# Kernel tuning notes

Hardware: AMD Instinct MI355X
Metric: run time of the kernel (lower is better)

Reference implementation:

```python
import jax, jax.numpy as jnp
import numpy as np

N, D, K = 8192, 512, 15  # points, embed dim, k_neighbors
EPS_MEAN = 1e-8
EPS_NORM = 1e-8


def _knn(emb, k):
    sq_norms = jnp.sum(emb * emb, axis=1)
    sq = sq_norms[:, None] + sq_norms[None, :] - 2.0 * (emb @ emb.T)
    sq = jnp.maximum(sq, 0.0)
    # smallest k+1 distances (squared dist is monotone in dist); slot 0 is self (dist 0)
    neg_vals, idx = jax.lax.top_k(-sq, k + 1)
    knn_sq = -neg_vals[:, 1:]
    knn_idx = idx[:, 1:]
    knn_d = jnp.sqrt(jnp.maximum(knn_sq, 1e-12))
    return knn_d, knn_idx


def _curvature_signature(knn_d):
    mean_d = jnp.mean(knn_d, axis=1, keepdims=True) + EPS_MEAN
    return jnp.sort(knn_d / mean_d, axis=1)


def _angular_signature(emb, knn_idx):
    k = knn_idx.shape[1]
    nb = emb[knn_idx]                      # [N, k, D] neighbor gather
    v = nb - emb[:, None, :]               # [N, k, D]
    nrm = jnp.linalg.norm(v, axis=2, keepdims=True)
    v = v / jnp.maximum(nrm, EPS_NORM)     # F.normalize semantics
    cos = jnp.einsum('nkd,nld->nkl', v, v)  # [N, k, k] batched small GEMM
    iu, ju = np.triu_indices(k, 1)
    ang = cos[:, iu, ju]                   # [N, k(k-1)/2]
    return jnp.sort(ang, axis=1)


def setup_inputs() -> dict:
    key = jax.random.key(0)
    k1, k2 = jax.random.split(key)
    embeddings = jax.random.normal(k1, (N, D), dtype=jnp.float32)
    # reference signatures computed from a perturbed copy (realistic set_reference)
    ref_emb = embeddings + 0.1 * jax.random.normal(k2, (N, D), dtype=jnp.float32)
    ref_d, ref_idx = _knn(ref_emb, K)
    reference_curvature_sig = _curvature_signature(ref_d)
    reference_angular_sig = _angular_signature(ref_emb, ref_idx)
    return {
        'embeddings': embeddings,
        'reference_curvature_sig': reference_curvature_sig,
        'reference_angular_sig': reference_angular_sig,
    }


def reference(embeddings, reference_curvature_sig, reference_angular_sig):
    n = embeddings.shape[0]
    k = min(K, n - 1)
    knn_d, knn_idx = _knn(embeddings, k)
    curr_curv = _curvature_signature(knn_d)          # [N, k]
    curr_ang = _angular_signature(embeddings, knn_idx)  # [N, k(k-1)/2]
    ref_curv = reference_curvature_sig[:n, :k]
    ref_ang = reference_angular_sig[:n]
    curv_loss = jnp.mean((curr_curv - ref_curv) ** 2)
    m = min(curr_ang.shape[1], ref_ang.shape[1])
    ang_loss = jnp.mean((curr_ang[:, :m] - ref_ang[:, :m]) ** 2)
    return 0.3 * curv_loss + 0.7 * ang_loss
```

## Files before the change

### kernel.cpp

```cpp
#include <hip/hip_runtime.h>
#include <hip/hip_bf16.h>
#include <math.h>

#define NPTS  8192
#define DIM   512
#define KNNK  15
#define NCAND 22
#define NPAIR 105
#define CINF  3.0e38f
#define EMPTYK 0xFFFFFFFFu
#define TAU_MARGIN (3u << 16)

#define NI      128
#define NJSPLIT 16
#define NJ      (NPTS/NJSPLIT)
#define JS      128
#define NSUB    (NJ/JS)
#define BK      32
#define NCH     (DIM/BK)
#define SDW     68
#define NLIST   NJSPLIT
#define NKEYS   (NLIST * KNNK)

#define BUF0_OFF   0
#define BUF1_OFF   16384
#define SQJ_OFF    34816
#define KNN_LDS    39936

typedef __attribute__((ext_vector_type(8))) short short8;
typedef __attribute__((ext_vector_type(4))) float f32x4;
typedef unsigned int uint32;

static __device__ __forceinline__ float wave_sum_f(float v) {
#pragma unroll
  for (int m = 32; m > 0; m >>= 1) v += __shfl_xor(v, m, 64);
  return v;
}

static __device__ __forceinline__ void load_lds16(const void* g, void* l) {
  __builtin_amdgcn_global_load_lds(
      (const __attribute__((address_space(1))) void*)g,
      (__attribute__((address_space(3))) void*)l, 16, 0, 0);
}

static __device__ __forceinline__ void bf16split(float x, short& h, short& l) {
  __hip_bfloat16 hb = __float2bfloat16(x);
  const float hf = __bfloat162float(hb);
  __hip_bfloat16 lb = __float2bfloat16(x - hf);
  h = *(short*)&hb;
  l = *(short*)&lb;
}

static __device__ __forceinline__ int lanes_below(unsigned long long B) {
  int c = __builtin_amdgcn_mbcnt_lo((uint32)B, 0);
  return __builtin_amdgcn_mbcnt_hi((uint32)(B >> 32), c);
}

static __device__ __forceinline__ void chain15(uint32 (&td)[15], uint32 c) {
#pragma unroll
  for (int p = 0; p < 15; ++p) {
    const uint32 lo = min(c, td[p]);
    const uint32 hi = max(c, td[p]);
    td[p] = lo; c = hi;
  }
}

#define PUSHK(k_) { const uint32 kv_ = (k_); \
  p0=(nc==0)?kv_:p0;  p1=(nc==1)?kv_:p1;  p2=(nc==2)?kv_:p2; \
  p3=(nc==3)?kv_:p3;  p4=(nc==4)?kv_:p4;  p5=(nc==5)?kv_:p5; \
  p6=(nc==6)?kv_:p6;  p7=(nc==7)?kv_:p7;  p8=(nc==8)?kv_:p8; \
  p9=(nc==9)?kv_:p9;  p10=(nc==10)?kv_:p10; p11=(nc==11)?kv_:p11; \
  ++nc; }

#define DRAINALL { \
  if (__any(nc >  0)) { if (nc >  0) chain15(td, p0);  } \
  if (__any(nc >  1)) { if (nc >  1) chain15(td, p1);  } \
  if (__any(nc >  2)) { if (nc >  2) chain15(td, p2);  } \
  if (__any(nc >  3)) { if (nc >  3) chain15(td, p3);  } \
  if (__any(nc >  4)) { if (nc >  4) chain15(td, p4);  } \
  if (__any(nc >  5)) { if (nc >  5) chain15(td, p5);  } \
  if (__any(nc >  6)) { if (nc >  6) chain15(td, p6);  } \
  if (__any(nc >  7)) { if (nc >  7) chain15(td, p7);  } \
  if (__any(nc >  8)) { if (nc >  8) chain15(td, p8);  } \
  if (__any(nc >  9)) { if (nc >  9) chain15(td, p9);  } \
  if (__any(nc > 10)) { if (nc > 10) chain15(td, p10); } \
  if (__any(nc > 11)) { if (nc > 11) chain15(td, p11); } \
  nc = 0; guard = min(tau_cur, td[14]); }

__global__ __launch_bounds__(256) void prep_kernel(
    const float* __restrict__ E, float* __restrict__ sqn,
    ushort* __restrict__ EA, ushort* __restrict__ EB,
    uint32* __restrict__ tauk) {
  const int row  = blockIdx.x * 4 + (threadIdx.x >> 6);
  const int lane = threadIdx.x & 63;
  const float SR2 = 1.4142135623730951f;
  float s = 0.f;
#pragma unroll
  for (int c = 0; c < 8; ++c) {
    const int d0 = lane + 64 * c;
    const float x = E[(size_t)row * DIM + d0];
    s = fmaf(x, x, s);
    __hip_bfloat16 ha = __float2bfloat16(-SR2 * x);
    __hip_bfloat16 hb = __float2bfloat16( SR2 * x);
    EA[(size_t)row * DIM + d0] = *(ushort*)&ha;
    EB[(size_t)row * DIM + d0] = *(ushort*)&hb;
  }
  s = wave_sum_f(s);
  if (lane == 0) { sqn[row] = s; tauk[row] = EMPTYK; }
}

__global__ __launch_bounds__(256, 4) void knn_kernel(
    const ushort* __restrict__ EA, const ushort* __restrict__ EB,
    const float* __restrict__ sqn, uint32* __restrict__ tauk,
    uint32* __restrict__ knnk) {
  __shared__ __align__(16) char sm[KNN_LDS];
  uint32* sdp  = (uint32*)sm;
  float*  sqjs = (float*)(sm + SQJ_OFF);

  const int tid = threadIdx.x;
  const int w   = tid >> 6;
  const int L   = tid & 63;
  const int wr  = (w >> 1) & 1;
  const int wc  = w & 1;
  const int i0  = blockIdx.x * NI;
  const int jsplit = blockIdx.y;
  const int j0  = jsplit * NJ;

  if (tid < NJ / 4) ((float4*)sqjs)[tid] = ((const float4*)(sqn + j0))[tid];

  const ushort* gsrc = (w < 2) ? EA : EB;
  const int lrow  = L >> 2;
  const int swz_k = ((L & 3) ^ ((L >> 3) & 3)) * 8;
  const int lds_woff = ((w < 2) ? 0 : 8192) + (w & 1) * 4096;
  const int slot8 = (((L >> 4) ^ ((L >> 1) & 3)) * 8);

  const int myrow = tid >> 1;
  const int h     = tid & 1;
  const int gi    = i0 + myrow;

  uint32 td[15];
#pragma unroll
  for (int p = 0; p < 15; ++p) td[p] = EMPTYK;

  __syncthreads();

  for (int js = 0; js < NSUB; ++js) {
    const int jrow0 = j0 + js * JS;
    const int trowW = ((w < 2) ? i0 : jrow0) + (w & 1) * 64;
    const ushort* gbase = gsrc + (size_t)(trowW + lrow) * DIM + swz_k;

    f32x4 acc[4][4];
#pragma unroll
    for (int fj = 0; fj < 4; ++fj) {
      const f32x4 sq = *(const f32x4*)&sqjs[js * 128 + wc * 64 + fj * 16 + (L >> 4) * 4];
#pragma unroll
      for (int fi = 0; fi < 4; ++fi) acc[fj][fi] = sq;
    }

    {
      char* lp = sm + BUF0_OFF + lds_woff;
#pragma unroll
      for (int s = 0; s < 4; ++s)
        load_lds16(gbase + (size_t)(s * 16) * DIM, lp + s * 1024);
    }
    __syncthreads();

#pragma unroll 2
    for (int ch = 0; ch < NCH; ++ch) {
      const int cb  = (ch & 1) ? BUF1_OFF : BUF0_OFF;
      const int nbo = (ch & 1) ? BUF0_OFF : BUF1_OFF;
      if (ch < NCH - 1) {
        char* lp = sm + nbo + lds_woff;
        const ushort* gp = gbase + (ch + 1) * BK;
#pragma unroll
        for (int s = 0; s < 4; ++s)
          load_lds16(gp + (size_t)(s * 16) * DIM, lp + s * 1024);
      }

      const ushort* sA = (const ushort*)(sm + cb);
      const ushort* sB = (const ushort*)(sm + cb + 8192);

      short8 a[4], b[4];
#pragma unroll
      for (int f = 0; f < 4; ++f) {
        a[f] = *(const short8*)&sA[(wr * 64 + f * 16 + (L & 15)) * BK + slot8];
        b[f] = *(const short8*)&sB[(wc * 64 + f * 16 + (L & 15)) * BK + slot8];
      }
#pragma unroll
      for (int fj = 0; fj < 4; ++fj)
#pragma unroll
        for (int fi = 0; fi < 4; ++fi)
          acc[fj][fi] = __builtin_amdgcn_mfma_f32_16x16x32_bf16(b[fj], a[fi], acc[fj][fi], 0, 0, 0);
      __syncthreads();
    }

#pragma unroll
    for (int fj = 0; fj < 4; ++fj)
#pragma unroll
      for (int fi = 0; fi < 4; ++fi) {
        const int i_t = wr * 64 + fi * 16 + (L & 15);
        const int jd  = wc * 32 + fj * 8 + (L >> 4) * 2;
        uint32 dw0, dw1;
        asm("v_cvt_pk_bf16_f32 %0, %1, %2" : "=v"(dw0) : "v"(acc[fj][fi][0]), "v"(acc[fj][fi][1]));
        asm("v_cvt_pk_bf16_f32 %0, %1, %2" : "=v"(dw1) : "v"(acc[fj][fi][2]), "v"(acc[fj][fi][3]));
        uint2 d2; d2.x = dw0; d2.y = dw1;
        *(uint2*)&sdp[i_t * SDW + jd] = d2;
      }
    __syncthreads();

    const uint32 tau_cur = __hip_atomic_load(&tauk[gi], __ATOMIC_RELAXED,
                                             __HIP_MEMORY_SCOPE_AGENT);
    const int selfc = gi - jrow0;
    if (selfc >= 0 && selfc < JS && h == (selfc >> 6))
      *(ushort*)(sm + myrow * (SDW * 4) + selfc * 2) = 0x7F80;

    const uint32* rowp = sdp + myrow * SDW + 32 * h;
    const uint32 jb = (uint32)(jrow0 + 64 * h);
    uint32 guard = min(tau_cur, td[14]);
    uint32 nc = 0;
    uint32 p0=0,p1=0,p2=0,p3=0,p4=0,p5=0,p6=0,p7=0,p8=0,p9=0,p10=0,p11=0;

#pragma unroll 2
    for (int q = 0; q < 8; ++q) {
      const uint4 pv = *(const uint4*)&rowp[4 * q];
      const uint32 jq = jb + 8 * q;
      uint32 kx;
      kx = (pv.x << 16)          | (jq + 0); if (kx < guard) PUSHK(kx);
      kx = (pv.x & 0xFFFF0000u)  | (jq + 1); if (kx < guard) PUSHK(kx);
      kx = (pv.y << 16)          | (jq + 2); if (kx < guard) PUSHK(kx);
      kx = (pv.y & 0xFFFF0000u)  | (jq + 3); if (kx < guard) PUSHK(kx);
      kx = (pv.z << 16)          | (jq + 4); if (kx < guard) PUSHK(kx);
      kx = (pv.z & 0xFFFF0000u)  | (jq + 5); if (kx < guard) PUSHK(kx);
      kx = (pv.w << 16)          | (jq + 6); if (kx < guard) PUSHK(kx);
      kx = (pv.w & 0xFFFF0000u)  | (jq + 7); if (kx < guard) PUSHK(kx);
      if (__any(nc >= 4)) { DRAINALL; }
    }
    if (__any(nc > 0)) { DRAINALL; }

    if (td[14] < 0x7F000000u) atomicMin(&tauk[gi], td[14] + TAU_MARGIN);
    __syncthreads();
  }

  uint32* mdk = (uint32*)sm;
#pragma unroll
  for (int p = 0; p < 15; ++p) mdk[(myrow * 2 + h) * 15 + p] = td[p];
  __syncthreads();
  if (h == 0) {
    const uint32* la = &mdk[(myrow * 2 + 0) * 15];
    const uint32* lb = &mdk[(myrow * 2 + 1) * 15];
    int pa = 0, pb = 0;
    const size_t base = ((size_t)gi * NLIST + jsplit) * KNNK;
    for (int s = 0; s < KNNK; ++s) {
      const uint32 va = la[pa], vb = lb[pb];
      uint32 v;
      if (va <= vb) { v = va; ++pa; } else { v = vb; ++pb; }
      knnk[base + s] = v;
    }
  }
}

__global__ __launch_bounds__(256) void sig_kernel(
    const float* __restrict__ E, const uint32* __restrict__ knnk,
    const float* __restrict__ refc, const float* __restrict__ refa,
    float2* __restrict__ pacc) {
  __shared__ float gsm[4][352];

  const int tid = threadIdx.x;
  const int wid = tid >> 6;
  const int L   = tid & 63;
  const int i   = blockIdx.x * 4 + wid;

  const uint32* kl = knnk + (size_t)i * NKEYS;
  const uint32 k0 = kl[L];
  const uint32 k1 = kl[L + 64];
  const uint32 k2 = kl[L + 128];
  const uint32 k3 = (L < NKEYS - 192) ? kl[L + 192] : EMPTYK;

  uint32 T = 0;
  for (int b = 31; b >= 0; --b) {
    const uint32 Tt = T | (1u << b);
    const int cnt = __popcll(__ballot(k0 < Tt)) + __popcll(__ballot(k1 < Tt)) +
                    __popcll(__ballot(k2 < Tt)) + __popcll(__ballot(k3 < Tt));
    if (cnt <= NCAND - 1) T = Tt;
  }

  uint32* candL = (uint32*)&gsm[wid][288];
  {
    const unsigned long long B0 = __ballot(k0 <= T);
    const unsigned long long B1 = __ballot(k1 <= T);
    const unsigned long long B2 = __ballot(k2 <= T);
    const unsigned long long B3 = __ballot(k3 <= T);
    int off = 0;
    if (k0 <= T) candL[off + lanes_below(B0)] = k0;
    off += __popcll(B0);
    if (k1 <= T) candL[off + lanes_below(B1)] = k1;
    off += __popcll(B1);
    if (k2 <= T) candL[off + lanes_below(B2)] = k2;
    off += __popcll(B2);
    if (k3 <= T) candL[off + lanes_below(B3)] = k3;
  }
  asm volatile("s_waitcnt lgkmcnt(0)" ::: "memory");
  const uint32 cand_key = (L < NCAND) ? candL[L] : EMPTYK;
  int cand_nb = ((cand_key >> 16) < 0x7F80u) ? (int)(cand_key & 0x1FFFu) : i;

  const float* Ei = E + (size_t)i * DIM;
  const int u = L & 7;
  const int g = L >> 3;
  float sr[3];
#pragma unroll
  for (int r = 0; r < 3; ++r) {
    const int c = r * 8 + g;
    const int row = __shfl(cand_nb, c, 64);
    const float4* r4 = (const float4*)(E + (size_t)row * DIM);
    const float4* e4 = (const float4*)Ei;
    float a0 = 0.f, a1 = 0.f, a2 = 0.f, a3 = 0.f;
#pragma unroll
    for (int t = 0; t < 16; ++t) {
      const float4 av = r4[u + 8 * t];
      const float4 ev = e4[u + 8 * t];
      const float d0 = av.x - ev.x, d1 = av.y - ev.y;
      const float d2 = av.z - ev.z, d3 = av.w - ev.w;
      a0 = fmaf(d0, d0, a0); a1 = fmaf(d1, d1, a1);
      a2 = fmaf(d2, d2, a2); a3 = fmaf(d3, d3, a3);
    }
    float s = (a0 + a1) + (a2 + a3);
    s += __shfl_xor(s, 1, 64);
    s += __shfl_xor(s, 2, 64);
    s += __shfl_xor(s, 4, 64);
    sr[r] = s;
  }
  const int srcl = (L & 7) * 8;
  const float t0 = __shfl(sr[0], srcl, 64);
  const float t1 = __shfl(sr[1], srcl, 64);
  const float t2 = __shfl(sr[2], srcl, 64);
  float csq = (L >> 3) == 0 ? t0 : ((L >> 3) == 1 ? t1 : t2);
  if (L >= NCAND || cand_nb == i) csq = CINF;

  int rank = 0;
#pragma unroll
  for (int j = 0; j < NCAND; ++j) {
    const float vj = __shfl(csq, j, 64);
    rank += (vj < csq) || (vj == csq && j < L);
  }
  float* dselL = &gsm[wid][312];
  int*   nbrL  = (int*)&gsm[wid][328];
  if (L < NCAND && rank < KNNK) { dselL[rank] = csq; nbrL[rank] = cand_nb; }
  asm volatile("s_waitcnt lgkmcnt(0)" ::: "memory");
  const int sel = L & 15;
  const int mynb = (sel < KNNK) ? nbrL[sel] : i;
  const float myd = (L < KNNK) ? sqrtf(fmaxf(dselL[L], 1e-12f)) : 0.f;

  float curvs;
  {
    float dd = (L < KNNK) ? myd : 0.f;
    float tot = wave_sum_f(dd);
    float mean_d = tot / (float)KNNK + 1e-8f;
    float diff = (L < KNNK) ? (dd / mean_d - refc[i * KNNK + L]) : 0.f;
    curvs = wave_sum_f(diff * diff);
  }

  const float4* nb4 = (const float4*)(E + (size_t)mynb * DIM);
  const float4* ei4 = (const float4*)Ei;
  const int qo = (L >> 4) * 2;

  f32x4 gH, gX1, gX2;
#pragma unroll
  for (int r = 0; r < 4; ++r) { gH[r] = 0.f; gX1[r] = 0.f; gX2[r] = 0.f; }

#pragma unroll
  for (int c = 0; c < 16; ++c) {
    const float4 f0 = nb4[qo + c * 8];
    const float4 f1 = nb4[qo + 1 + c * 8];
    const float4 g0 = ei4[qo + c * 8];
    const float4 g1 = ei4[qo + 1 + c * 8];
    float v[8];
    v[0] = f0.x - g0.x; v[1] = f0.y - g0.y; v[2] = f0.z - g0.z; v[3] = f0.w - g0.w;
    v[4] = f1.x - g1.x; v[5] = f1.y - g1.y; v[6] = f1.z - g1.z; v[7] = f1.w - g1.w;
    short8 ah, al;
#pragma unroll
    for (int q = 0; q < 8; ++q) {
      short hh, ll;
      bf16split(v[q], hh, ll);
      ah[q] = hh; al[q] = ll;
    }
    gH  = __builtin_amdgcn_mfma_f32_16x16x32_bf16(ah, ah, gH, 0, 0, 0);
    gX1 = __builtin_amdgcn_mfma_f32_16x16x32_bf16(ah, al, gX1, 0, 0, 0);
    gX2 = __builtin_amdgcn_mfma_f32_16x16x32_bf16(al, ah, gX2, 0, 0, 0);
  }

#pragma unroll
  for (int q = 0; q < 4; ++q)
    gsm[wid][((L >> 4) * 4 + q) * 17 + (L & 15)] = gH[q] + gX1[q] + gX2[q];
  asm volatile("s_waitcnt lgkmcnt(0)" ::: "memory");

  if (L < 16) {
    const float dv = gsm[wid][L * 17 + L];
    const float nrm = sqrtf(fmaxf(dv, 0.f));
    gsm[wid][272 + L] = 1.0f / fmaxf(nrm, 1e-8f);
  }
  asm volatile("s_waitcnt lgkmcnt(0)" ::: "memory");

  float c0 = CINF, c1 = CINF;
#pragma unroll
  for (int s = 0; s < 2; ++s) {
    const int p = L + 64 * s;
    if (p < NPAIR) {
      int a = 0, rem = p, cnt = 14;
      while (rem >= cnt) { rem -= cnt; --cnt; ++a; }
      const int b = a + 1 + rem;
      const float cv = gsm[wid][a * 17 + b] * gsm[wid][272 + a] * gsm[wid][272 + b];
      if (s == 0) c0 = cv; else c1 = cv;
    }
  }

#pragma unroll
  for (int k = 2; k <= 128; k <<= 1) {
#pragma unroll
    for (int j = k >> 1; j >= 1; j >>= 1) {
      const bool dir = ((L & (k >> 1)) == 0);
      if (j == 1) {
        const float lo = fminf(c0, c1), hi = fmaxf(c0, c1);
        c0 = dir ? lo : hi;
        c1 = dir ? hi : lo;
      } else {
        const int m = j >> 1;
        const float o0 = __shfl_xor(c0, m, 64);
        const float o1 = __shfl_xor(c1, m, 64);
        const bool lower = ((L & m) == 0);
        c0 = (lower == dir) ? fminf(c0, o0) : fmaxf(c0, o0);
        c1 = (lower == dir) ? fminf(c1, o1) : fmaxf(c1, o1);
      }
    }
  }

  float part = 0.f;
  {
    const int r0 = 2 * L, r1 = 2 * L + 1;
    if (r0 < NPAIR) { const float dd = c0 - refa[(size_t)i * NPAIR + r0]; part += dd * dd; }
    if (r1 < NPAIR) { const float dd = c1 - refa[(size_t)i * NPAIR + r1]; part += dd * dd; }
  }
  part = wave_sum_f(part);
  if (L == 0) pacc[i] = make_float2(curvs, part);
}

__global__ __launch_bounds__(256) void fin_kernel(
    const float2* __restrict__ pacc, float* __restrict__ out) {
  __shared__ double redc[4], reda[4];
  const int tid = threadIdx.x;
  const int wid = tid >> 6;
  const int L   = tid & 63;
  double sc = 0.0, sa = 0.0;
#pragma unroll
  for (int q = 0; q < 32; ++q) {
    const float2 p = pacc[tid + 256 * q];
    sc += (double)p.x;
    sa += (double)p.y;
  }
#pragma unroll
  for (int m = 32; m > 0; m >>= 1) {
    sc += __shfl_xor(sc, m, 64);
    sa += __shfl_xor(sa, m, 64);
  }
  if (L == 0) { redc[wid] = sc; reda[wid] = sa; }
  __syncthreads();
  if (tid == 0) {
    const double curv = (redc[0] + redc[1] + redc[2] + redc[3]) /
                        ((double)NPTS * (double)KNNK);
    const double ang  = (reda[0] + reda[1] + reda[2] + reda[3]) /
                        ((double)NPTS * (double)NPAIR);
    out[0] = (float)(0.3 * curv + 0.7 * ang);
  }
}

extern "C" void kernel_launch(void* const* d_in, const int* in_sizes, int n_in,
                              void* d_out, int out_size, void* d_ws,
                              size_t ws_size, hipStream_t stream) {
  const float* E    = (const float*)d_in[0];
  const float* refc = (const float*)d_in[1];
  const float* refa = (const float*)d_in[2];
  float* out = (float*)d_out;

  char* ws = (char*)d_ws;
  float*  sqn  = (float*)(ws + 1024);
  float2* pacc = (float2*)(ws + 65536);
  uint32* tauk = (uint32*)(ws + 131072);
  ushort* EA   = (ushort*)(ws + 1048576);
  ushort* EB   = (ushort*)(ws + 9437184);
  uint32* knnk = (uint32*)(ws + 17825792);

  prep_kernel<<<NPTS / 4, 256, 0, stream>>>(E, sqn, EA, EB, tauk);
  knn_kernel<<<dim3(NPTS / NI, NJSPLIT), 256, 0, stream>>>(EA, EB, sqn, tauk, knnk);
  sig_kernel<<<NPTS / 4, 256, 0, stream>>>(E, knnk, refc, refa, pacc);
  fin_kernel<<<1, 256, 0, stream>>>(pacc, out);
}
```

Before: 277.9 us.

## Switch KNN distance GEMM from bf16 to int8 MFMA with quantized embeddings

Embeddings are quantized to int8 (scale 32, clamped) in the prep kernel, and the candidate distance GEMM uses the i32 16x16x64 int8 MFMA instead of bf16 16x16x32. This halves operand bytes and doubles K per MFMA. It also uses integer half-squared norms as the accumulator init. To compensate for the coarser screening precision, the candidate count and tau margin are widened. Exact rescoring later presumably keeps results correct, but quantization may miss true neighbors if the margin is insufficient.

```diff
diff --git a/kernel.cpp b/kernel.cpp
--- a/kernel.cpp
+++ b/kernel.cpp
@@ -5,19 +5,19 @@
 #define NPTS  8192
 #define DIM   512
 #define KNNK  15
-#define NCAND 22
+#define NCAND 24
 #define NPAIR 105
 #define CINF  3.0e38f
 #define EMPTYK 0xFFFFFFFFu
-#define TAU_MARGIN (3u << 16)
+#define TAU_MARGIN (6u << 16)
 
 #define NI      128
 #define NJSPLIT 16
 #define NJ      (NPTS/NJSPLIT)
 #define JS      128
 #define NSUB    (NJ/JS)
-#define BK      32
-#define NCH     (DIM/BK)
+#define BKB     64
+#define NCH     (DIM/BKB)
 #define SDW     68
 #define NLIST   NJSPLIT
 #define NKEYS   (NLIST * KNNK)
@@ -27,8 +27,7 @@
 #define SQJ_OFF    34816
 #define KNN_LDS    39936
 
-typedef __attribute__((ext_vector_type(8))) short short8;
-typedef __attribute__((ext_vector_type(4))) float f32x4;
+typedef __attribute__((ext_vector_type(4))) int i32x4;
 typedef unsigned int uint32;
 
 static __device__ __forceinline__ float wave_sum_f(float v) {
@@ -88,34 +87,43 @@
   nc = 0; guard = min(tau_cur, td[14]); }
 
 __global__ __launch_bounds__(256) void prep_kernel(
-    const float* __restrict__ E, float* __restrict__ sqn,
-    ushort* __restrict__ EA, ushort* __restrict__ EB,
+    const float* __restrict__ E, int* __restrict__ sqnh,
+    unsigned char* __restrict__ EA, unsigned char* __restrict__ EB,
     uint32* __restrict__ tauk) {
   const int row  = blockIdx.x * 4 + (threadIdx.x >> 6);
   const int lane = threadIdx.x & 63;
-  const float SR2 = 1.4142135623730951f;
-  float s = 0.f;
-#pragma unroll
-  for (int c = 0; c < 8; ++c) {
-    const int d0 = lane + 64 * c;
-    const float x = E[(size_t)row * DIM + d0];
-    s = fmaf(x, x, s);
-    __hip_bfloat16 ha = __float2bfloat16(-SR2 * x);
-    __hip_bfloat16 hb = __float2bfloat16( SR2 * x);
-    EA[(size_t)row * DIM + d0] = *(ushort*)&ha;
-    EB[(size_t)row * DIM + d0] = *(ushort*)&hb;
-  }
-  s = wave_sum_f(s);
-  if (lane == 0) { sqn[row] = s; tauk[row] = EMPTYK; }
+  const float4* e4 = (const float4*)(E + (size_t)row * DIM);
+  const float4 f0 = e4[lane * 2];
+  const float4 f1 = e4[lane * 2 + 1];
+  const float xs[8] = {f0.x, f0.y, f0.z, f0.w, f1.x, f1.y, f1.z, f1.w};
+  int ss = 0;
+  uint32 pa0 = 0, pa1 = 0, pb0 = 0, pb1 = 0;
+#pragma unroll
+  for (int t = 0; t < 8; ++t) {
+    const float v = fminf(fmaxf(xs[t] * 32.0f, -127.0f), 127.0f);
+    const int q = __float2int_rn(v);
+    ss += q * q;
+    const uint32 ub = (uint32)(q & 0xFF);
+    const uint32 ua = (uint32)((-q) & 0xFF);
+    if (t < 4) { pb0 |= ub << (8 * t);       pa0 |= ua << (8 * t); }
+    else       { pb1 |= ub << (8 * (t - 4)); pa1 |= ua << (8 * (t - 4)); }
+  }
+  uint2 wa; wa.x = pa0; wa.y = pa1;
+  uint2 wb; wb.x = pb0; wb.y = pb1;
+  ((uint2*)(EA + (size_t)row * DIM))[lane] = wa;
+  ((uint2*)(EB + (size_t)row * DIM))[lane] = wb;
+#pragma unroll
+  for (int m = 32; m > 0; m >>= 1) ss += __shfl_xor(ss, m, 64);
+  if (lane == 0) { sqnh[row] = ss >> 1; tauk[row] = EMPTYK; }
 }
 
 __global__ __launch_bounds__(256, 4) void knn_kernel(
-    const ushort* __restrict__ EA, const ushort* __restrict__ EB,
-    const float* __restrict__ sqn, uint32* __restrict__ tauk,
+    const unsigned char* __restrict__ EA, const unsigned char* __restrict__ EB,
+    const int* __restrict__ sqnh, uint32* __restrict__ tauk,
     uint32* __restrict__ knnk) {
   __shared__ __align__(16) char sm[KNN_LDS];
   uint32* sdp  = (uint32*)sm;
-  float*  sqjs = (float*)(sm + SQJ_OFF);
+  int*    sqji = (int*)(sm + SQJ_OFF);
 
   const int tid = threadIdx.x;
   const int w   = tid >> 6;
@@ -126,13 +134,13 @@
   const int jsplit = blockIdx.y;
   const int j0  = jsplit * NJ;
 
-  if (tid < NJ / 4) ((float4*)sqjs)[tid] = ((const float4*)(sqn + j0))[tid];
-
-  const ushort* gsrc = (w < 2) ? EA : EB;
-  const int lrow  = L >> 2;
-  const int swz_k = ((L & 3) ^ ((L >> 3) & 3)) * 8;
+  if (tid < NJ / 4) ((int4*)sqji)[tid] = ((const int4*)(sqnh + j0))[tid];
+
+  const unsigned char* gsrc = (w < 2) ? EA : EB;
+  const int lrow   = L >> 2;
+  const int swz_kB = ((L & 3) ^ ((L >> 3) & 3)) * 16;
   const int lds_woff = ((w < 2) ? 0 : 8192) + (w & 1) * 4096;
-  const int slot8 = (((L >> 4) ^ ((L >> 1) & 3)) * 8);
+  const int slotB  = (((L >> 4) ^ ((L >> 1) & 3)) * 16);
 
   const int myrow = tid >> 1;
   const int h     = tid & 1;
@@ -147,12 +155,12 @@
   for (int js = 0; js < NSUB; ++js) {
     const int jrow0 = j0 + js * JS;
     const int trowW = ((w < 2) ? i0 : jrow0) + (w & 1) * 64;
-    const ushort* gbase = gsrc + (size_t)(trowW + lrow) * DIM + swz_k;
-
-    f32x4 acc[4][4];
+    const unsigned char* gbase = gsrc + (size_t)(trowW + lrow) * DIM + swz_kB;
+
+    i32x4 acc[4][4];
 #pragma unroll
     for (int fj = 0; fj < 4; ++fj) {
-      const f32x4 sq = *(const f32x4*)&sqjs[js * 128 + wc * 64 + fj * 16 + (L >> 4) * 4];
+      const i32x4 sq = *(const i32x4*)&sqji[js * 128 + wc * 64 + fj * 16 + (L >> 4) * 4];
 #pragma unroll
       for (int fi = 0; fi < 4; ++fi) acc[fj][fi] = sq;
     }
@@ -171,26 +179,26 @@
       const int nbo = (ch & 1) ? BUF0_OFF : BUF1_OFF;
       if (ch < NCH - 1) {
         char* lp = sm + nbo + lds_woff;
-        const ushort* gp = gbase + (ch + 1) * BK;
+        const unsigned char* gp = gbase + (ch + 1) * BKB;
 #pragma unroll
         for (int s = 0; s < 4; ++s)
           load_lds16(gp + (size_t)(s * 16) * DIM, lp + s * 1024);
       }
 
-      const ushort* sA = (const ushort*)(sm + cb);
-      const ushort* sB = (const ushort*)(sm + cb + 8192);
-
-      short8 a[4], b[4];
+      const char* sA = (const char*)(sm + cb);
+      const char* sB = (const char*)(sm + cb + 8192);
+
+      i32x4 a[4], b[4];
 #pragma unroll
       for (int f = 0; f < 4; ++f) {
-        a[f] = *(const short8*)&sA[(wr * 64 + f * 16 + (L & 15)) * BK + slot8];
-        b[f] = *(const short8*)&sB[(wc * 64 + f * 16 + (L & 15)) * BK + slot8];
+        a[f] = *(const i32x4*)&sA[(wr * 64 + f * 16 + (L & 15)) * BKB + slotB];
+        b[f] = *(const i32x4*)&sB[(wc * 64 + f * 16 + (L & 15)) * BKB + slotB];
       }
 #pragma unroll
       for (int fj = 0; fj < 4; ++fj)
 #pragma unroll
         for (int fi = 0; fi < 4; ++fi)
-          acc[fj][fi] = __builtin_amdgcn_mfma_f32_16x16x32_bf16(b[fj], a[fi], acc[fj][fi], 0, 0, 0);
+          acc[fj][fi] = __builtin_amdgcn_mfma_i32_16x16x64_i8(b[fj], a[fi], acc[fj][fi], 0, 0, 0);
       __syncthreads();
     }
 
@@ -200,9 +208,13 @@
       for (int fi = 0; fi < 4; ++fi) {
         const int i_t = wr * 64 + fi * 16 + (L & 15);
         const int jd  = wc * 32 + fj * 8 + (L >> 4) * 2;
+        const float v0 = (float)acc[fj][fi][0];
+        const float v1 = (float)acc[fj][fi][1];
+        const float v2 = (float)acc[fj][fi][2];
+        const float v3 = (float)acc[fj][fi][3];
         uint32 dw0, dw1;
-        asm("v_cvt_pk_bf16_f32 %0, %1, %2" : "=v"(dw0) : "v"(acc[fj][fi][0]), "v"(acc[fj][fi][1]));
-        asm("v_cvt_pk_bf16_f32 %0, %1, %2" : "=v"(dw1) : "v"(acc[fj][fi][2]), "v"(acc[fj][fi][3]));
+        asm("v_cvt_pk_bf16_f32 %0, %1, %2" : "=v"(dw0) : "v"(v0), "v"(v1));
+        asm("v_cvt_pk_bf16_f32 %0, %1, %2" : "=v"(dw1) : "v"(v2), "v"(v3));
         uint2 d2; d2.x = dw0; d2.y = dw1;
         *(uint2*)&sdp[i_t * SDW + jd] = d2;
       }
@@ -363,6 +375,8 @@
   const float4* ei4 = (const float4*)Ei;
   const int qo = (L >> 4) * 2;
 
+  typedef __attribute__((ext_vector_type(8))) short short8;
+  typedef __attribute__((ext_vector_type(4))) float f32x4;
   f32x4 gH, gX1, gX2;
 #pragma unroll
   for (int r = 0; r < 4; ++r) { gH[r] = 0.f; gX1[r] = 0.f; gX2[r] = 0.f; }
@@ -481,15 +495,15 @@
   float* out = (float*)d_out;
 
   char* ws = (char*)d_ws;
-  float*  sqn  = (float*)(ws + 1024);
+  int*    sqnh = (int*)(ws + 1024);
   float2* pacc = (float2*)(ws + 65536);
   uint32* tauk = (uint32*)(ws + 131072);
-  ushort* EA   = (ushort*)(ws + 1048576);
-  ushort* EB   = (ushort*)(ws + 9437184);
+  unsigned char* EA = (unsigned char*)(ws + 1048576);
+  unsigned char* EB = (unsigned char*)(ws + 9437184);
   uint32* knnk = (uint32*)(ws + 17825792);
 
-  prep_kernel<<<NPTS / 4, 256, 0, stream>>>(E, sqn, EA, EB, tauk);
-  knn_kernel<<<dim3(NPTS / NI, NJSPLIT), 256, 0, stream>>>(EA, EB, sqn, tauk, knnk);
+  prep_kernel<<<NPTS / 4, 256, 0, stream>>>(E, sqnh, EA, EB, tauk);
+  knn_kernel<<<dim3(NPTS / NI, NJSPLIT), 256, 0, stream>>>(EA, EB, sqnh, tauk, knnk);
   sig_kernel<<<NPTS / 4, 256, 0, stream>>>(E, knnk, refc, refa, pacc);
   fin_kernel<<<1, 256, 0, stream>>>(pacc, out);
 }
```

Result: faster. 260.5 us (-6.2%).
